# Optimization experiments

Measured on AMD Instinct MI355X. Metric: run time of the kernel, lower is better.

Reference implementation:

```python
import jax, jax.numpy as jnp
import numpy as np

B, C, N, K = 2, 128, 4096, 16
DIM, PH, AH = 256, 64, 1024  # dim, pos_hidden_dim, dim*attn_hidden_multiplier
EPS = 1e-5

def _p(k, shape, scale=0.02):
    return jax.random.normal(k, shape, dtype=jnp.float32) * scale

def setup_inputs() -> dict:
    key0 = jax.random.key(0)
    ks = jax.random.split(key0, 32)
    d = {
        'pos': jax.random.normal(ks[0], (B, 3, N), dtype=jnp.float32),
        'key': jax.random.normal(ks[1], (B, C, N), dtype=jnp.float32),
        'query': jax.random.normal(ks[2], (B, C, N), dtype=jnp.float32),
        # MLP_Res on concat(key,query): in=2C, hidden=C, out=C
        'mlpv_w1': _p(ks[3], (C, 2 * C)), 'mlpv_b1': jnp.zeros((C,)),
        'mlpv_w2': _p(ks[4], (C, C)),     'mlpv_b2': jnp.zeros((C,)),
        'mlpv_ws': _p(ks[5], (C, 2 * C)), 'mlpv_bs': jnp.zeros((C,)),
        'wk': _p(ks[6], (DIM, C)), 'bk': jnp.zeros((DIM,)),
        'wq': _p(ks[7], (DIM, C)), 'bq': jnp.zeros((DIM,)),
        'wv': _p(ks[8], (DIM, C)), 'bv': jnp.zeros((DIM,)),
        # pos_mlp: Conv2d(3,PH,1) -> BN -> ReLU -> Conv2d(PH,DIM,1)
        'pos_w1': _p(ks[9], (PH, 3)),   'pos_b1': jnp.zeros((PH,)),
        'pos_g1': jnp.ones((PH,)),      'pos_be1': jnp.zeros((PH,)),
        'pos_w2': _p(ks[10], (DIM, PH)),'pos_b2': jnp.zeros((DIM,)),
        # attn_mlp: Conv2d(DIM,AH,1) -> BN -> ReLU -> Conv2d(AH,DIM,1)
        'att_w1': _p(ks[11], (AH, DIM)), 'att_b1': jnp.zeros((AH,)),
        'att_g1': jnp.ones((AH,)),       'att_be1': jnp.zeros((AH,)),
        'att_w2': _p(ks[12], (DIM, AH)), 'att_b2': jnp.zeros((DIM,)),
        'we': _p(ks[13], (C, DIM)), 'be': jnp.zeros((C,)),
    }
    return d

def conv1d(w, b, x):  # 1x1 conv: (o,i),(B,i,N)->(B,o,N)
    return jnp.einsum('oi,bin->bon', w, x) + b[None, :, None]

def conv2d(w, b, x):  # 1x1 conv: (o,i),(B,i,N,K)->(B,o,N,K)
    return jnp.einsum('oi,bink->bonk', w, x) + b[None, :, None, None]

def bn2d(g, be, x):  # training-mode batchnorm over (B,N,K) per channel
    m = x.mean(axis=(0, 2, 3), keepdims=True)
    v = x.var(axis=(0, 2, 3), keepdims=True)
    return g[None, :, None, None] * (x - m) * jax.lax.rsqrt(v + EPS) + be[None, :, None, None]

def knn_idx(pos, k):  # pos: (B,3,N) -> idx (B,N,k) of k nearest (incl. self)
    sq = jnp.sum(pos * pos, axis=1)                      # (B,N)
    d2 = sq[:, :, None] + sq[:, None, :] - 2.0 * jnp.einsum('bdn,bdm->bnm', pos, pos)
    _, idx = jax.lax.top_k(-d2, k)                       # smallest distances
    return idx

def group(x, idx):  # x:(B,C,N), idx:(B,N,K) -> (B,C,N,K)
    return jax.vmap(lambda xb, ib: xb[:, ib])(x, idx)

def reference(pos, key, query,
              mlpv_w1, mlpv_b1, mlpv_w2, mlpv_b2, mlpv_ws, mlpv_bs,
              wk, bk, wq, bq, wv, bv,
              pos_w1, pos_b1, pos_g1, pos_be1, pos_w2, pos_b2,
              att_w1, att_b1, att_g1, att_be1, att_w2, att_b2,
              we, be):
    x = jnp.concatenate([key, query], axis=1)            # (B,2C,N)
    value = conv1d(mlpv_w2, mlpv_b2, jax.nn.relu(conv1d(mlpv_w1, mlpv_b1, x))) \
            + conv1d(mlpv_ws, mlpv_bs, x)                # MLP_Res -> (B,C,N)
    identity = value
    k_f = conv1d(wk, bk, key)                            # (B,DIM,N)
    q_f = conv1d(wq, bq, query)
    v_f = conv1d(wv, bv, value)
    idx = knn_idx(pos, K)                                # (B,N,K)
    key_g = group(k_f, idx)                              # (B,DIM,N,K)
    qk_rel = q_f[:, :, :, None] - key_g
    pos_rel = pos[:, :, :, None] - group(pos, idx)       # (B,3,N,K)
    pos_emb = conv2d(pos_w2, pos_b2,
                     jax.nn.relu(bn2d(pos_g1, pos_be1, conv2d(pos_w1, pos_b1, pos_rel))))
    attn = conv2d(att_w2, att_b2,
                  jax.nn.relu(bn2d(att_g1, att_be1, conv2d(att_w1, att_b1, qk_rel + pos_emb))))
    attn = jax.nn.softmax(attn, axis=-1)                 # softmax over K neighbors
    v = v_f[:, :, :, None] + pos_emb                     # (B,DIM,N,K)
    agg = jnp.einsum('bcik,bcik->bci', attn, v)          # (B,DIM,N)
    y = conv1d(we, be, agg)
    return y + identity
```

## Files before the change

### kernel.cpp

```cpp
#include <hip/hip_runtime.h>
#include <math.h>

#define BB 2
#define CC 128
#define NN 4096
#define KK 16
#define DIMD 256
#define PHH 64
#define AHH 1024
#define EPSF 1e-5f
#define RSPLIT 128
#define RKCH ((BB * NN * KK) / RSPLIT)
#define LSTR 258
#define KNN_CAP 512
#define FPT 8

typedef unsigned short ushort_t;
typedef unsigned char uchar_t;
typedef unsigned long long u64;
typedef long long i64;
typedef __attribute__((ext_vector_type(8))) short short8;
typedef __attribute__((ext_vector_type(8))) unsigned short u16x8;
typedef __attribute__((ext_vector_type(4))) unsigned short u16x4;
typedef __attribute__((ext_vector_type(2))) unsigned short u16x2;
typedef __attribute__((ext_vector_type(4))) float f32x4;

__device__ __forceinline__ ushort_t f2b(float x) {
    union { float f; unsigned u; } v; v.f = x;
    unsigned r = v.u + 0x7fff + ((v.u >> 16) & 1);
    return (ushort_t)(r >> 16);
}
__device__ __forceinline__ float b2f(ushort_t x) {
    union { unsigned u; float f; } v; v.u = ((unsigned)x) << 16;
    return v.f;
}
__device__ __forceinline__ unsigned fsort(float x) {
    union { float f; unsigned u; } v; v.f = x;
    return v.u ^ ((v.u >> 31) ? 0xFFFFFFFFu : 0x80000000u);
}
__device__ __forceinline__ uchar_t f2f8(float x) {
    int p = __builtin_amdgcn_cvt_pk_fp8_f32(x, x, 0, false);
    return (uchar_t)(p & 0xFF);
}

#define GLDS16(gp, lp) __builtin_amdgcn_global_load_lds( \
    (const __attribute__((address_space(1))) void*)(gp), \
    (__attribute__((address_space(3))) void*)(lp), 16, 0, 0)

__global__ void zero_kernel(float* p, int n) {
    int i = blockIdx.x * blockDim.x + threadIdx.x;
    if (i < n) p[i] = 0.f;
}

__global__ __launch_bounds__(256) void knn_kernel(const float* __restrict__ pos,
                                                  int* __restrict__ idx) {
    int bid = blockIdx.x;
    int b = bid / NN, n = bid % NN;
    int t = threadIdx.x;
    int lane = t & 63, w = t >> 6;
    const float* px = pos + (size_t)b * 3 * NN;
    const float* py = px + NN;
    const float* pz = px + 2 * NN;
    float qx = px[n], qy = py[n], qz = pz[n];
    float qs = qx * qx + qy * qy + qz * qz;

    u64 keys[KK];
    u64 lmin = ~0ull;
#pragma unroll
    for (int j = 0; j < KK; ++j) {
        int m = t + 256 * j;
        float mx = px[m], my = py[m], mz = pz[m];
        float ms = mx * mx + my * my + mz * mz;
        float dt = qx * mx + qy * my + qz * mz;
        float d = qs + ms - 2.f * dt;
        u64 k = ((u64)fsort(d) << 32) | (unsigned)m;
        keys[j] = k;
        lmin = k < lmin ? k : lmin;
    }

    __shared__ u64 T0s[4];
    __shared__ u64 pool[KNN_CAP];
    __shared__ int cnt;

    u64 k = lmin, m4 = 0;
#pragma unroll
    for (int r = 0; r < 4; ++r) {
        u64 mv = k;
#pragma unroll
        for (int off = 32; off >= 1; off >>= 1) {
            u64 o = __shfl_xor(mv, off);
            mv = o < mv ? o : mv;
        }
        if (r == 3) m4 = mv;
        if (k == mv) k = ~0ull;
    }
    if (lane == 0) T0s[w] = m4;
    if (t == 0) cnt = 0;
    __syncthreads();
    u64 T0 = T0s[0];
    T0 = T0s[1] > T0 ? T0s[1] : T0;
    T0 = T0s[2] > T0 ? T0s[2] : T0;
    T0 = T0s[3] > T0 ? T0s[3] : T0;

#pragma unroll
    for (int j = 0; j < KK; ++j) {
        if (keys[j] <= T0) {
            int p = atomicAdd(&cnt, 1);
            if (p < KNN_CAP) pool[p] = keys[j];
        }
    }
    __syncthreads();
    int C = cnt < KNN_CAP ? cnt : KNN_CAP;
    if (t < C) {
        u64 me = pool[t];
        int r = 0;
        for (int i = 0; i < C; ++i) r += (pool[i] < me);
        if (r < KK) idx[(size_t)bid * KK + r] = (int)(me & 0xFFFFFFFFu);
    }
}

__global__ __launch_bounds__(256) void cvtx_kernel(const float* __restrict__ key,
                                                   const float* __restrict__ query,
                                                   ushort_t* __restrict__ kqT) {
    __shared__ float xs[128][65];
    int b = blockIdx.y, n0 = blockIdx.x * 64, t = threadIdx.x;
    for (int h = 0; h < 2; ++h) {
        const float* src = (h ? query : key) + (size_t)b * CC * NN;
        if (h) __syncthreads();
#pragma unroll
        for (int it = 0; it < 32; ++it) {
            int l = it * 256 + t;
            xs[l >> 6][l & 63] = src[(size_t)(l >> 6) * NN + n0 + (l & 63)];
        }
        __syncthreads();
#pragma unroll
        for (int it = 0; it < 8; ++it) {
            int l = it * 256 + t;
            int row = l >> 5, c0 = (l & 31) * 4;
            u16x4 pk;
            pk[0] = f2b(xs[c0][row]);
            pk[1] = f2b(xs[c0 + 1][row]);
            pk[2] = f2b(xs[c0 + 2][row]);
            pk[3] = f2b(xs[c0 + 3][row]);
            *(u16x4*)(kqT + ((size_t)b * NN + n0 + row) * 256 + h * 128 + c0) = pk;
        }
    }
}

template <int KLOOP, int ASTR, int EPI, int OSTR>
__global__ __launch_bounds__(256) void gemmT_kernel(const ushort_t* __restrict__ A,
                                                    const ushort_t* __restrict__ Bm,
                                                    const float* __restrict__ bias,
                                                    float* __restrict__ outF,
                                                    ushort_t* __restrict__ outB) {
    __shared__ ushort_t lA[128 * 32];
    __shared__ ushort_t lB[128 * 32];
    int t = threadIdx.x, lane = t & 63, w = t >> 6;
    int wr = w >> 1, wc = w & 1;
    size_t row0 = (size_t)blockIdx.x * 128;
    int col0 = blockIdx.y * 128;
    int m16 = lane & 15, kg = lane >> 4;
    f32x4 acc[4][4];
#pragma unroll
    for (int i = 0; i < 4; ++i)
#pragma unroll
        for (int j = 0; j < 4; ++j) acc[i][j] = (f32x4){0.f, 0.f, 0.f, 0.f};

    const ushort_t* gA = A + (row0 + (size_t)w * 16 + m16) * ASTR + kg * 8;
    const ushort_t* gB = Bm + ((size_t)(col0 + w * 16 + m16)) * KLOOP + kg * 8;
    ushort_t* lA0 = lA + w * 512;
    ushort_t* lB0 = lB + w * 512;
    for (int kt = 0; kt < KLOOP / 32; ++kt) {
        int ko = kt * 32;
        GLDS16(gA + ko, lA0);
        GLDS16(gA + (size_t)64 * ASTR + ko, lA0 + 2048);
        GLDS16(gB + ko, lB0);
        GLDS16(gB + (size_t)64 * KLOOP + ko, lB0 + 2048);
        __syncthreads();
        short8 af[4], bf[4];
#pragma unroll
        for (int i = 0; i < 4; ++i) {
            af[i] = *(const short8*)(lA + ((wr * 4 + i) * 512 + kg * 128 + m16 * 8));
            bf[i] = *(const short8*)(lB + ((wc * 4 + i) * 512 + kg * 128 + m16 * 8));
        }
#pragma unroll
        for (int i = 0; i < 4; ++i)
#pragma unroll
            for (int j = 0; j < 4; ++j)
                acc[i][j] = __builtin_amdgcn_mfma_f32_16x16x32_bf16(af[i], bf[j], acc[i][j], 0, 0, 0);
        __syncthreads();
    }
#pragma unroll
    for (int j = 0; j < 4; ++j) {
        int n = col0 + wc * 64 + j * 16 + m16;
        float bi = bias[n];
#pragma unroll
        for (int i = 0; i < 4; ++i) {
            size_t r = row0 + wr * 64 + i * 16 + kg * 4;
#pragma unroll
            for (int rg = 0; rg < 4; ++rg) {
                float v = acc[i][j][rg] + bi;
                if (EPI == 0) outB[(r + rg) * (size_t)OSTR + n] = f2b(fmaxf(v, 0.f));
                else          outF[(r + rg) * (size_t)OSTR + n] = v;
            }
        }
    }
}

__global__ __launch_bounds__(256) void gemmval_kernel(const ushort_t* __restrict__ kqT,
                                                      const ushort_t* __restrict__ h1T,
                                                      const ushort_t* __restrict__ wsb,
                                                      const ushort_t* __restrict__ w2vb,
                                                      const float* __restrict__ b2,
                                                      const float* __restrict__ bs,
                                                      float* __restrict__ valueTf,
                                                      ushort_t* __restrict__ valueTb) {
    __shared__ ushort_t lA[128 * 32];
    __shared__ ushort_t lB[128 * 32];
    int t = threadIdx.x, lane = t & 63, w = t >> 6;
    int wr = w >> 1, wc = w & 1;
    size_t row0 = (size_t)blockIdx.x * 128;
    int m16 = lane & 15, kg = lane >> 4;
    f32x4 acc[4][4];
#pragma unroll
    for (int i = 0; i < 4; ++i)
#pragma unroll
        for (int j = 0; j < 4; ++j) acc[i][j] = (f32x4){0.f, 0.f, 0.f, 0.f};
    ushort_t* lA0 = lA + w * 512;
    ushort_t* lB0 = lB + w * 512;

    {
        const ushort_t* gA = kqT + (row0 + (size_t)w * 16 + m16) * 256 + kg * 8;
        const ushort_t* gB = wsb + ((size_t)(w * 16 + m16)) * 256 + kg * 8;
        for (int kt = 0; kt < 8; ++kt) {
            int ko = kt * 32;
            GLDS16(gA + ko, lA0);
            GLDS16(gA + (size_t)64 * 256 + ko, lA0 + 2048);
            GLDS16(gB + ko, lB0);
            GLDS16(gB + (size_t)64 * 256 + ko, lB0 + 2048);
            __syncthreads();
            short8 af[4], bf[4];
#pragma unroll
            for (int i = 0; i < 4; ++i) {
                af[i] = *(const short8*)(lA + ((wr * 4 + i) * 512 + kg * 128 + m16 * 8));
                bf[i] = *(const short8*)(lB + ((wc * 4 + i) * 512 + kg * 128 + m16 * 8));
            }
#pragma unroll
            for (int i = 0; i < 4; ++i)
#pragma unroll
                for (int j = 0; j < 4; ++j)
                    acc[i][j] = __builtin_amdgcn_mfma_f32_16x16x32_bf16(af[i], bf[j], acc[i][j], 0, 0, 0);
            __syncthreads();
        }
    }
    {
        const ushort_t* gA = h1T + (row0 + (size_t)w * 16 + m16) * 128 + kg * 8;
        const ushort_t* gB = w2vb + ((size_t)(w * 16 + m16)) * 128 + kg * 8;
        for (int kt = 0; kt < 4; ++kt) {
            int ko = kt * 32;
            GLDS16(gA + ko, lA0);
            GLDS16(gA + (size_t)64 * 128 + ko, lA0 + 2048);
            GLDS16(gB + ko, lB0);
            GLDS16(gB + (size_t)64 * 128 + ko, lB0 + 2048);
            __syncthreads();
            short8 af[4], bf[4];
#pragma unroll
            for (int i = 0; i < 4; ++i) {
                af[i] = *(const short8*)(lA + ((wr * 4 + i) * 512 + kg * 128 + m16 * 8));
                bf[i] = *(const short8*)(lB + ((wc * 4 + i) * 512 + kg * 128 + m16 * 8));
            }
#pragma unroll
            for (int i = 0; i < 4; ++i)
#pragma unroll
                for (int j = 0; j < 4; ++j)
                    acc[i][j] = __builtin_amdgcn_mfma_f32_16x16x32_bf16(af[i], bf[j], acc[i][j], 0, 0, 0);
            __syncthreads();
        }
    }
#pragma unroll
    for (int j = 0; j < 4; ++j) {
        int n = wc * 64 + j * 16 + m16;
        float bi = b2[n] + bs[n];
#pragma unroll
        for (int i = 0; i < 4; ++i) {
            size_t r = row0 + wr * 64 + i * 16 + kg * 4;
#pragma unroll
            for (int rg = 0; rg < 4; ++rg) {
                float v = acc[i][j][rg] + bi;
                valueTf[(r + rg) * (size_t)CC + n] = v;
                valueTb[(r + rg) * (size_t)CC + n] = f2b(v);
            }
        }
    }
}

__global__ __launch_bounds__(256) void gemmkq_kernel(const ushort_t* __restrict__ kqT,
                                                     const ushort_t* __restrict__ wkb,
                                                     const ushort_t* __restrict__ wqb,
                                                     const float* __restrict__ bk,
                                                     const float* __restrict__ bq,
                                                     float* __restrict__ kT,
                                                     float* __restrict__ qT) {
    __shared__ ushort_t lA[128 * 32];
    __shared__ ushort_t lB[128 * 32];
    int half = blockIdx.y >> 1;
    int col0 = (blockIdx.y & 1) * 128;
    const ushort_t* A = kqT + half * 128;
    const ushort_t* Bm = half ? wqb : wkb;
    const float* bias = half ? bq : bk;
    float* outF = half ? qT : kT;

    int t = threadIdx.x, lane = t & 63, w = t >> 6;
    int wr = w >> 1, wc = w & 1;
    size_t row0 = (size_t)blockIdx.x * 128;
    int m16 = lane & 15, kg = lane >> 4;
    f32x4 acc[4][4];
#pragma unroll
    for (int i = 0; i < 4; ++i)
#pragma unroll
        for (int j = 0; j < 4; ++j) acc[i][j] = (f32x4){0.f, 0.f, 0.f, 0.f};
    const ushort_t* gA = A + (row0 + (size_t)w * 16 + m16) * 256 + kg * 8;
    const ushort_t* gB = Bm + ((size_t)(col0 + w * 16 + m16)) * 128 + kg * 8;
    ushort_t* lA0 = lA + w * 512;
    ushort_t* lB0 = lB + w * 512;
    for (int kt = 0; kt < 4; ++kt) {
        int ko = kt * 32;
        GLDS16(gA + ko, lA0);
        GLDS16(gA + (size_t)64 * 256 + ko, lA0 + 2048);
        GLDS16(gB + ko, lB0);
        GLDS16(gB + (size_t)64 * 128 + ko, lB0 + 2048);
        __syncthreads();
        short8 af[4], bf[4];
#pragma unroll
        for (int i = 0; i < 4; ++i) {
            af[i] = *(const short8*)(lA + ((wr * 4 + i) * 512 + kg * 128 + m16 * 8));
            bf[i] = *(const short8*)(lB + ((wc * 4 + i) * 512 + kg * 128 + m16 * 8));
        }
#pragma unroll
        for (int i = 0; i < 4; ++i)
#pragma unroll
            for (int j = 0; j < 4; ++j)
                acc[i][j] = __builtin_amdgcn_mfma_f32_16x16x32_bf16(af[i], bf[j], acc[i][j], 0, 0, 0);
        __syncthreads();
    }
#pragma unroll
    for (int j = 0; j < 4; ++j) {
        int n = col0 + wc * 64 + j * 16 + m16;
        float bi = bias[n];
#pragma unroll
        for (int i = 0; i < 4; ++i) {
            size_t r = row0 + wr * 64 + i * 16 + kg * 4;
#pragma unroll
            for (int rg = 0; rg < 4; ++rg)
                outF[(r + rg) * (size_t)DIMD + n] = acc[i][j][rg] + bi;
        }
    }
}

__global__ __launch_bounds__(256) void pos_stats_kernel(const float* __restrict__ pos,
                                                        const int* __restrict__ idx,
                                                        float* __restrict__ stats) {
    int sid = blockIdx.x * 256 + threadIdx.x;
    int b = sid / (NN * KK);
    int r = sid % (NN * KK);
    int n = r / KK;
    int m = idx[sid];
    const float* px = pos + (size_t)b * 3 * NN;
    float dx = px[n] - px[m];
    float dy = px[NN + n] - px[NN + m];
    float dz = px[2 * NN + n] - px[2 * NN + m];
    float v[9] = {dx, dy, dz, dx * dx, dy * dy, dz * dz, dx * dy, dx * dz, dy * dz};
    __shared__ float red[256];
    for (int j = 0; j < 9; ++j) {
        red[threadIdx.x] = v[j];
        __syncthreads();
        for (int off = 128; off >= 1; off >>= 1) {
            if (threadIdx.x < off) red[threadIdx.x] += red[threadIdx.x + off];
            __syncthreads();
        }
        if (threadIdx.x == 0) atomicAdd(&stats[j], red[0]);
        __syncthreads();
    }
}

__global__ void pos_bn_kernel(const float* __restrict__ stats, const float* __restrict__ pw1,
                              const float* __restrict__ pb1, const float* __restrict__ pg1,
                              const float* __restrict__ pbe1, float* __restrict__ posA) {
    int c = threadIdx.x;
    if (c >= PHH) return;
    float M = (float)(BB * NN * KK);
    float mu0 = stats[0] / M, mu1 = stats[1] / M, mu2 = stats[2] / M;
    float E00 = stats[3] / M, E11 = stats[4] / M, E22 = stats[5] / M;
    float E01 = stats[6] / M, E02 = stats[7] / M, E12 = stats[8] / M;
    float w0 = pw1[c * 3], w1 = pw1[c * 3 + 1], w2 = pw1[c * 3 + 2];
    float wmu = w0 * mu0 + w1 * mu1 + w2 * mu2;
    float mean_h = wmu + pb1[c];
    float Eh2 = w0 * w0 * E00 + w1 * w1 * E11 + w2 * w2 * E22
              + 2.f * (w0 * w1 * E01 + w0 * w2 * E02 + w1 * w2 * E12)
              + 2.f * pb1[c] * wmu + pb1[c] * pb1[c];
    float var = Eh2 - mean_h * mean_h;
    float a1 = pg1[c] * rsqrtf(var + EPSF);
    posA[c] = a1;
    posA[PHH + c] = pbe1[c] - mean_h * a1;
}

__global__ __launch_bounds__(256) void p1_kernel(const float* __restrict__ pos,
                                                 const int* __restrict__ idx,
                                                 const float* __restrict__ pw1,
                                                 const float* __restrict__ pb1,
                                                 const float* __restrict__ posA,
                                                 ushort_t* __restrict__ p1) {
    int gid = blockIdx.x * 256 + threadIdx.x;
    int samp = gid >> 6, c = gid & 63;
    int p = samp >> 4;
    int b = p >> 12, n = p & (NN - 1);
    int m = idx[samp];
    const float* px = pos + (size_t)b * 3 * NN;
    float dx = px[n] - px[m];
    float dy = px[NN + n] - px[NN + m];
    float dz = px[2 * NN + n] - px[2 * NN + m];
    float h = pw1[c * 3] * dx + pw1[c * 3 + 1] * dy + pw1[c * 3 + 2] * dz + pb1[c];
    p1[gid] = f2b(fmaxf(h * posA[c] + posA[PHH + c], 0.f));
}

__global__ __launch_bounds__(256) void mu_kernel(const ushort_t* __restrict__ sb16,
                                                 float* __restrict__ mu) {
    __shared__ float red[8][DIMD];
    int t = threadIdx.x;
    int rg = t >> 5;
    int c0 = (t & 31) * 8;
    const ushort_t* p = sb16 + ((size_t)blockIdx.x * 512 + rg * 64) * DIMD + c0;
    float a0 = 0.f, a1 = 0.f, a2 = 0.f, a3 = 0.f, a4 = 0.f, a5 = 0.f, a6 = 0.f, a7 = 0.f;
    for (int i = 0; i < 64; ++i) {
        u16x8 v = *(const u16x8*)(p + (size_t)i * DIMD);
        a0 += b2f(v[0]); a1 += b2f(v[1]); a2 += b2f(v[2]); a3 += b2f(v[3]);
        a4 += b2f(v[4]); a5 += b2f(v[5]); a6 += b2f(v[6]); a7 += b2f(v[7]);
    }
    red[rg][c0] = a0; red[rg][c0 + 1] = a1; red[rg][c0 + 2] = a2; red[rg][c0 + 3] = a3;
    red[rg][c0 + 4] = a4; red[rg][c0 + 5] = a5; red[rg][c0 + 6] = a6; red[rg][c0 + 7] = a7;
    __syncthreads();
    float s = 0.f;
#pragma unroll
    for (int g = 0; g < 8; ++g) s += red[g][t];
    atomicAdd(&mu[t], s);
}

__global__ __launch_bounds__(256) void rg_kernel(const ushort_t* __restrict__ S,
                                                 float* __restrict__ Rpart) {
    __shared__ ushort_t ls[32 * LSTR];
    int t = threadIdx.x;
    int lane = t & 63, w = t >> 6;
    int wr = w >> 1, wc = w & 1;
    int ti = blockIdx.y >> 1, tj = blockIdx.y & 1;
    int m16 = lane & 15, kg = lane >> 4;
    size_t kbase = (size_t)blockIdx.x * RKCH;

    f32x4 acc[4][4];
#pragma unroll
    for (int i = 0; i < 4; ++i)
#pragma unroll
        for (int j = 0; j < 4; ++j) acc[i][j] = (f32x4){0.f, 0.f, 0.f, 0.f};

    int lm = t >> 3;
    int lc = (t & 7) * 32;
    const ushort_t* gS = S + (kbase + lm) * DIMD + lc;
    ushort_t* lp = ls + lm * LSTR + lc;

    for (int kt = 0; kt < RKCH / 32; ++kt) {
        const ushort_t* gp = gS + (size_t)kt * 32 * DIMD;
        u16x8 v0 = *(const u16x8*)(gp);
        u16x8 v1 = *(const u16x8*)(gp + 8);
        u16x8 v2 = *(const u16x8*)(gp + 16);
        u16x8 v3 = *(const u16x8*)(gp + 24);
        __syncthreads();
#pragma unroll
        for (int q = 0; q < 4; ++q) {
            *(u16x2*)(lp + 0 + 2 * q) = (u16x2){v0[2 * q], v0[2 * q + 1]};
            *(u16x2*)(lp + 8 + 2 * q) = (u16x2){v1[2 * q], v1[2 * q + 1]};
            *(u16x2*)(lp + 16 + 2 * q) = (u16x2){v2[2 * q], v2[2 * q + 1]};
            *(u16x2*)(lp + 24 + 2 * q) = (u16x2){v3[2 * q], v3[2 * q + 1]};
        }
        __syncthreads();
        short8 af[4], bf[4];
#pragma unroll
        for (int i = 0; i < 4; ++i) {
            int chA = ti * 128 + wr * 64 + i * 16 + m16;
            int chB = tj * 128 + wc * 64 + i * 16 + m16;
#pragma unroll
            for (int j = 0; j < 8; ++j) {
                int k = kg * 8 + j;
                af[i][j] = (short)ls[k * LSTR + chA];
                bf[i][j] = (short)ls[k * LSTR + chB];
            }
        }
#pragma unroll
        for (int i = 0; i < 4; ++i)
#pragma unroll
            for (int j = 0; j < 4; ++j)
                acc[i][j] = __builtin_amdgcn_mfma_f32_16x16x32_bf16(af[i], bf[j], acc[i][j], 0, 0, 0);
    }

    float* rp = Rpart + (size_t)blockIdx.x * (DIMD * DIMD);
#pragma unroll
    for (int i = 0; i < 4; ++i) {
        int r0 = ti * 128 + wr * 64 + i * 16 + kg * 4;
#pragma unroll
        for (int j = 0; j < 4; ++j) {
            int cn = tj * 128 + wc * 64 + j * 16 + m16;
#pragma unroll
            for (int rg = 0; rg < 4; ++rg)
                rp[(size_t)(r0 + rg) * DIMD + cn] = acc[i][j][rg];
        }
    }
}

__global__ __launch_bounds__(256) void r_reduce_kernel(const float* __restrict__ Rpart,
                                                       float* __restrict__ R) {
    int e = blockIdx.x * 256 + threadIdx.x;
    float s = 0.f;
    for (int p = 0; p < RSPLIT; ++p) s += Rpart[(size_t)p * (DIMD * DIMD) + e];
    R[e] = s;
}

__global__ __launch_bounds__(256) void attn_bn_kernel(const float* __restrict__ R,
                                                      const float* __restrict__ mu,
                                                      const float* __restrict__ aw1,
                                                      const float* __restrict__ ab1,
                                                      const float* __restrict__ ag1,
                                                      const float* __restrict__ abe1,
                                                      float* __restrict__ attA) {
    int c = blockIdx.x;
    int t = threadIdx.x;
    __shared__ float wsh[DIMD];
    __shared__ float red[DIMD];
    wsh[t] = aw1[(size_t)c * DIMD + t];
    __syncthreads();
    const float* Rr = R + (size_t)t * DIMD;
    float q = 0.f;
#pragma unroll 4
    for (int j = 0; j < DIMD; ++j) q += Rr[j] * wsh[j];
    red[t] = q * wsh[t];
    __syncthreads();
    for (int off = 128; off >= 1; off >>= 1) {
        if (t < off) red[t] += red[t + off];
        __syncthreads();
    }
    float wRw = red[0];
    __syncthreads();
    red[t] = wsh[t] * mu[t];
    __syncthreads();
    for (int off = 128; off >= 1; off >>= 1) {
        if (t < off) red[t] += red[t + off];
        __syncthreads();
    }
    if (t == 0) {
        float M = (float)(BB * NN * KK);
        float wmu = red[0] / M;
        float b1c = ab1[c];
        float Eh = wmu + b1c;
        float Eh2 = wRw / M + 2.f * b1c * wmu + b1c * b1c;
        float var = Eh2 - Eh * Eh;
        float a1 = ag1[c] * rsqrtf(var + EPSF);
        attA[c] = a1;
        attA[AHH + c] = a1 * b1c + abe1[c] - Eh * a1;
    }
}

__global__ void cvt_w_kernel(const float* __restrict__ aw1, const float* __restrict__ aw2,
                             const float* __restrict__ pw2,
                             const float* __restrict__ mw1, const float* __restrict__ mws,
                             const float* __restrict__ mw2,
                             const float* __restrict__ wk, const float* __restrict__ wq,
                             const float* __restrict__ wv,
                             ushort_t* __restrict__ w1b, ushort_t* __restrict__ w2b,
                             ushort_t* __restrict__ pw2b,
                             ushort_t* __restrict__ w1vb, ushort_t* __restrict__ wsvb,
                             ushort_t* __restrict__ w2vb,
                             ushort_t* __restrict__ wkb, ushort_t* __restrict__ wqb,
                             ushort_t* __restrict__ wvb,
                             uchar_t* __restrict__ w2f8) {
    int i = blockIdx.x * 256 + threadIdx.x;
    int o = i;
    if (o < 262144) { w1b[o] = f2b(aw1[o]); return; }   o -= 262144;
    if (o < 262144) { w2b[o] = f2b(aw2[o]); w2f8[o] = f2f8(aw2[o] * 64.f); return; } o -= 262144;
    if (o < 16384)  { pw2b[o] = f2b(pw2[o]); return; }  o -= 16384;
    if (o < 32768)  { w1vb[o] = f2b(mw1[o]); return; }  o -= 32768;
    if (o < 32768)  { wsvb[o] = f2b(mws[o]); return; }  o -= 32768;
    if (o < 16384)  { w2vb[o] = f2b(mw2[o]); return; }  o -= 16384;
    if (o < 32768)  { wkb[o] = f2b(wk[o]); return; }    o -= 32768;
    if (o < 32768)  { wqb[o] = f2b(wq[o]); return; }    o -= 32768;
    if (o < 32768)  { wvb[o] = f2b(wv[o]); }
}

template <int KDIM>
__global__ __launch_bounds__(256) void gemmS_kernel(const ushort_t* __restrict__ A,
                                                    const ushort_t* __restrict__ Bm,
                                                    const float* __restrict__ p0,
                                                    ushort_t* __restrict__ Sb,
                                                    const float* __restrict__ qT,
                                                    const float* __restrict__ kT,
                                                    const int* __restrict__ gidx) {
    __shared__ ushort_t lA[128 * 32];
    __shared__ ushort_t lB[128 * 32];
    int t = threadIdx.x;
    int lane = t & 63, w = t >> 6;
    int wr = w >> 1, wc = w & 1;
    size_t row0 = (size_t)blockIdx.x * 128;
    int col0 = blockIdx.y * 128;
    int m16 = lane & 15, kg = lane >> 4;

    f32x4 acc[4][4];
#pragma unroll
    for (int i = 0; i < 4; ++i)
#pragma unroll
        for (int j = 0; j < 4; ++j) acc[i][j] = (f32x4){0.f, 0.f, 0.f, 0.f};

    const ushort_t* gA = A + (row0 + (size_t)w * 16 + m16) * KDIM + kg * 8;
    const ushort_t* gB = Bm + ((size_t)(col0 + w * 16 + m16)) * KDIM + kg * 8;
    ushort_t* lA0 = lA + w * 512;
    ushort_t* lB0 = lB + w * 512;

    for (int kt = 0; kt < KDIM / 32; ++kt) {
        int ko = kt * 32;
        GLDS16(gA + ko, lA0);
        GLDS16(gA + (size_t)64 * KDIM + ko, lA0 + 2048);
        GLDS16(gB + ko, lB0);
        GLDS16(gB + (size_t)64 * KDIM + ko, lB0 + 2048);
        __syncthreads();
        short8 af[4], bf[4];
#pragma unroll
        for (int i = 0; i < 4; ++i) {
            af[i] = *(const short8*)(lA + ((wr * 4 + i) * 512 + kg * 128 + m16 * 8));
            bf[i] = *(const short8*)(lB + ((wc * 4 + i) * 512 + kg * 128 + m16 * 8));
        }
#pragma unroll
        for (int i = 0; i < 4; ++i)
#pragma unroll
            for (int j = 0; j < 4; ++j)
                acc[i][j] = __builtin_amdgcn_mfma_f32_16x16x32_bf16(af[i], bf[j], acc[i][j], 0, 0, 0);
        __syncthreads();
    }

    int nn[4]; float bi[4];
#pragma unroll
    for (int j = 0; j < 4; ++j) { nn[j] = col0 + wc * 64 + j * 16 + m16; bi[j] = p0[nn[j]]; }
#pragma unroll
    for (int i = 0; i < 4; ++i) {
        size_t r = row0 + wr * 64 + i * 16 + kg * 4;
#pragma unroll
        for (int rg = 0; rg < 4; ++rg) {
            size_t rr = r + rg;
            int p = (int)(rr >> 4);
            int krow = (p & ~(NN - 1)) + gidx[rr];
            const float* qrow = qT + (size_t)p * DIMD;
            const float* kro = kT + (size_t)krow * DIMD;
#pragma unroll
            for (int j = 0; j < 4; ++j) {
                float sv = qrow[nn[j]] - kro[nn[j]] + acc[i][j][rg] + bi[j];
                Sb[rr * (size_t)DIMD + nn[j]] = f2b(sv);
            }
        }
    }
}

__global__ __launch_bounds__(256, 3) void fused_mlp_kernel(const ushort_t* __restrict__ S,
                                                        const ushort_t* __restrict__ w1b,
                                                        const uchar_t* __restrict__ w2f8,
                                                        const float* __restrict__ attA,
                                                        const float* __restrict__ ab2,
                                                        const int* __restrict__ idx,
                                                        const float* __restrict__ qT,
                                                        const float* __restrict__ kT,
                                                        const float* __restrict__ vT,
                                                        float* __restrict__ aggT) {
    __shared__ char smem[49152];
    ushort_t* lS  = (ushort_t*)smem;
    uchar_t*  lHt = (uchar_t*)(smem + 32768);
    ushort_t* lgB = (ushort_t*)smem;

    int t = threadIdx.x;
    int lane = t & 63, w = t >> 6;
    int m16 = lane & 15, kg = lane >> 4;
    size_t row0 = (size_t)blockIdx.x * 64;

#pragma unroll
    for (int i = 0; i < 8; ++i) {
        int lb = w * 8 + i;
        int kt = lb >> 2, st = lb & 3;
        const ushort_t* gp = S + (row0 + st * 16 + m16) * DIMD + kt * 32 + kg * 8;
        GLDS16(gp, lS + lb * 512);
    }

    f32x4 acc2[4][4];
#pragma unroll
    for (int i = 0; i < 4; ++i)
#pragma unroll
        for (int j = 0; j < 4; ++j) acc2[i][j] = (f32x4){0.f, 0.f, 0.f, 0.f};

    __syncthreads();

    for (int jc = 0; jc < 8; ++jc) {
        uchar_t* lHb = lHt + (jc & 1) * 8192;
        f32x4 acc1[2][4];
#pragma unroll
        for (int hi = 0; hi < 2; ++hi)
#pragma unroll
            for (int sj = 0; sj < 4; ++sj) acc1[hi][sj] = (f32x4){0.f, 0.f, 0.f, 0.f};
        const ushort_t* wrow = w1b + ((size_t)(jc * 128 + w * 32 + m16)) * DIMD + kg * 8;
#pragma unroll
        for (int kt = 0; kt < 8; ++kt) {
            short8 af[2], bf[4];
            af[0] = *(const short8*)(wrow + kt * 32);
            af[1] = *(const short8*)(wrow + (size_t)16 * DIMD + kt * 32);
#pragma unroll
            for (int sj = 0; sj < 4; ++sj)
                bf[sj] = *(const short8*)(lS + (kt * 4 + sj) * 512 + kg * 128 + m16 * 8);
            __builtin_amdgcn_s_setprio(1);
#pragma unroll
            for (int hi = 0; hi < 2; ++hi)
#pragma unroll
                for (int sj = 0; sj < 4; ++sj)
                    acc1[hi][sj] = __builtin_amdgcn_mfma_f32_16x16x32_bf16(af[hi], bf[sj], acc1[hi][sj], 0, 0, 0);
            __builtin_amdgcn_s_setprio(0);
        }
#pragma unroll
        for (int hi = 0; hi < 2; ++hi) {
            float4 sc4 = *(const float4*)(attA + jc * 128 + w * 32 + hi * 16 + kg * 4);
            float4 of4 = *(const float4*)(attA + AHH + jc * 128 + w * 32 + hi * 16 + kg * 4);
#pragma unroll
            for (int sj = 0; sj < 4; ++sj) {
                float h0 = fmaxf(sc4.x * acc1[hi][sj][0] + of4.x, 0.f);
                float h1 = fmaxf(sc4.y * acc1[hi][sj][1] + of4.y, 0.f);
                float h2 = fmaxf(sc4.z * acc1[hi][sj][2] + of4.z, 0.f);
                float h3 = fmaxf(sc4.w * acc1[hi][sj][3] + of4.w, 0.f);
                int p01 = __builtin_amdgcn_cvt_pk_fp8_f32(h0, h1, 0, false);
                int pk = __builtin_amdgcn_cvt_pk_fp8_f32(h2, h3, p01, true);
                int ah = (w * 4 + sj) * 512 + (hi * 2 + (kg >> 1)) * 128 + m16 * 8 + (kg & 1) * 4;
                *(int*)(lHb + ah) = pk;
            }
        }
        __syncthreads();
#pragma unroll
        for (int gh = 0; gh < 2; ++gh) {
            i64 af2[8];
#pragma unroll
            for (int gq = 0; gq < 2; ++gq)
#pragma unroll
                for (int oi = 0; oi < 4; ++oi)
                    af2[gq * 4 + oi] = *(const i64*)(w2f8 + ((size_t)(w * 64 + oi * 16 + m16)) * AHH + jc * 128 + (gh * 2 + gq) * 32 + kg * 8);
#pragma unroll
            for (int gq = 0; gq < 2; ++gq) {
                i64 bf2[4];
#pragma unroll
                for (int sj = 0; sj < 4; ++sj)
                    bf2[sj] = *(const i64*)(lHb + ((gh * 2 + gq) * 4 + sj) * 512 + kg * 128 + m16 * 8);
                __builtin_amdgcn_s_setprio(1);
#pragma unroll
                for (int oi = 0; oi < 4; ++oi)
#pragma unroll
                    for (int sj = 0; sj < 4; ++sj)
                        acc2[oi][sj] = __builtin_amdgcn_mfma_f32_16x16x32_fp8_fp8(af2[gq * 4 + oi], bf2[sj], acc2[oi][sj], 0, 0, 0);
                __builtin_amdgcn_s_setprio(0);
            }
        }
    }
    __syncthreads();

    const float invsc = 0.015625f;
#pragma unroll
    for (int oi = 0; oi < 4; ++oi) {
        int ob = w * 64 + oi * 16 + kg * 4;
        float4 b2v = *(const float4*)(ab2 + ob);
#pragma unroll
        for (int sj = 0; sj < 4; ++sj) {
            int smp = sj * 16 + m16;
            lgB[(ob + 0) * 72 + smp] = f2b(acc2[oi][sj][0] * invsc + b2v.x);
            lgB[(ob + 1) * 72 + smp] = f2b(acc2[oi][sj][1] * invsc + b2v.y);
            lgB[(ob + 2) * 72 + smp] = f2b(acc2[oi][sj][2] * invsc + b2v.z);
            lgB[(ob + 3) * 72 + smp] = f2b(acc2[oi][sj][3] * invsc + b2v.w);
        }
    }
    __syncthreads();

    int out = t;
    for (int pt = 0; pt < 4; ++pt) {
        int pid = (int)(row0 >> 4) + pt;
        u16x8 v0 = *(const u16x8*)(lgB + out * 72 + pt * 16);
        u16x8 v1 = *(const u16x8*)(lgB + out * 72 + pt * 16 + 8);
        float lg[KK];
#pragma unroll
        for (int s = 0; s < 8; ++s) { lg[s] = b2f(v0[s]); lg[s + 8] = b2f(v1[s]); }
        float mx = lg[0];
#pragma unroll
        for (int s = 1; s < KK; ++s) mx = fmaxf(mx, lg[s]);
        float se = 0.f;
#pragma unroll
        for (int s = 0; s < KK; ++s) { lg[s] = expf(lg[s] - mx); se += lg[s]; }
        float inv = 1.f / se;
        int base = pid & ~(NN - 1);
        float acc = 0.f;
#pragma unroll
        for (int s = 0; s < KK; ++s) {
            int row = pid * KK + s;
            int krow = base + idx[row];
            float sv = b2f(S[(size_t)row * DIMD + out]);
            float kv = kT[(size_t)krow * DIMD + out];
            acc += lg[s] * (sv + kv);
        }
        float vf = vT[(size_t)pid * DIMD + out];
        float q  = qT[(size_t)pid * DIMD + out];
        aggT[(size_t)pid * DIMD + out] = vf - q + acc * inv;
    }
}

__global__ __launch_bounds__(256) void final_kernel(const float* __restrict__ aggT,
                                                    const float* __restrict__ we,
                                                    const float* __restrict__ be,
                                                    const float* __restrict__ valueTf,
                                                    float* __restrict__ out) {
    __shared__ float xs[2 * FPT][DIMD];
    __shared__ float vs[2 * FPT][CC];
    int b = blockIdx.y;
    int n0 = blockIdx.x * (2 * FPT);
    int t = threadIdx.x;
    const float4* src = (const float4*)(aggT + ((size_t)b * NN + n0) * DIMD);
    float4* dst = (float4*)xs;
#pragma unroll
    for (int l = 0; l < (2 * FPT * DIMD / 4) / 256; ++l) dst[t + 256 * l] = src[t + 256 * l];
    const float4* src2 = (const float4*)(valueTf + ((size_t)b * NN + n0) * CC);
    float4* dst2 = (float4*)vs;
#pragma unroll
    for (int l = 0; l < (2 * FPT * CC / 4) / 256; ++l) dst2[t + 256 * l] = src2[t + 256 * l];
    __syncthreads();
    int o = t & 127, ph = t >> 7;
    float acc[FPT];
#pragma unroll
    for (int p = 0; p < FPT; ++p) acc[p] = 0.f;
    const float4* wr = (const float4*)(we + (size_t)o * DIMD);
#pragma unroll 8
    for (int i4 = 0; i4 < DIMD / 4; ++i4) {
        float4 w4 = wr[i4];
#pragma unroll
        for (int p = 0; p < FPT; ++p) {
            float4 x4 = *(const float4*)&xs[ph * FPT + p][i4 * 4];
            acc[p] += w4.x * x4.x + w4.y * x4.y + w4.z * x4.z + w4.w * x4.w;
        }
    }
    float bo = be[o];
#pragma unroll
    for (int p = 0; p < FPT; ++p) {
        size_t oi = ((size_t)b * CC + o) * NN + n0 + ph * FPT + p;
        out[oi] = acc[p] + bo + vs[ph * FPT + p][o];
    }
}

extern "C" void kernel_launch(void* const* d_in, const int* in_sizes, int n_in,
                              void* d_out, int out_size, void* d_ws, size_t ws_size,
                              hipStream_t stream) {
    (void)in_sizes; (void)n_in; (void)out_size; (void)ws_size;
    const float* pos     = (const float*)d_in[0];
    const float* key     = (const float*)d_in[1];
    const float* query   = (const float*)d_in[2];
    const float* mlpv_w1 = (const float*)d_in[3];
    const float* mlpv_b1 = (const float*)d_in[4];
    const float* mlpv_w2 = (const float*)d_in[5];
    const float* mlpv_b2 = (const float*)d_in[6];
    const float* mlpv_ws = (const float*)d_in[7];
    const float* mlpv_bs = (const float*)d_in[8];
    const float* wk  = (const float*)d_in[9];
    const float* bk  = (const float*)d_in[10];
    const float* wq  = (const float*)d_in[11];
    const float* bq  = (const float*)d_in[12];
    const float* wv  = (const float*)d_in[13];
    const float* bv  = (const float*)d_in[14];
    const float* pw1 = (const float*)d_in[15];
    const float* pb1 = (const float*)d_in[16];
    const float* pg1 = (const float*)d_in[17];
    const float* pbe1= (const float*)d_in[18];
    const float* pw2 = (const float*)d_in[19];
    const float* pb2 = (const float*)d_in[20];
    const float* aw1 = (const float*)d_in[21];
    const float* ab1 = (const float*)d_in[22];
    const float* ag1 = (const float*)d_in[23];
    const float* abe1= (const float*)d_in[24];
    const float* aw2 = (const float*)d_in[25];
    const float* ab2 = (const float*)d_in[26];
    const float* we  = (const float*)d_in[27];
    const float* be  = (const float*)d_in[28];
    float* out = (float*)d_out;

    char* wsb = (char*)d_ws;
    size_t off = 0;
    auto alloc = [&](size_t bytes) {
        void* p = wsb + off;
        off += (bytes + 255) & ~(size_t)255;
        return p;
    };
    const size_t M = (size_t)BB * NN * KK;
    const size_t P = (size_t)BB * NN;
    int*   idx   = (int*)  alloc(M * 4);
    ushort_t* kqT     = (ushort_t*)alloc(P * 256 * 2);
    ushort_t* h1T     = (ushort_t*)alloc(P * CC * 2);
    float*    valueTf = (float*)   alloc(P * CC * 4);
    ushort_t* valueTb = (ushort_t*)alloc(P * CC * 2);
    float* kT    = (float*)alloc(P * DIMD * 4);
    float* qT    = (float*)alloc(P * DIMD * 4);
    float* vT    = (float*)alloc(P * DIMD * 4);
    float* aggT  = (float*)alloc(P * DIMD * 4);
    float* zero0 = (float*)alloc((size_t)(16 + 256 + 65536) * 4);
    float* stats = zero0;
    float* mu    = zero0 + 16;
    float* R     = zero0 + 16 + 256;
    float* posA  = (float*)alloc((size_t)2 * PHH * 4);
    float* attA  = (float*)alloc((size_t)2 * AHH * 4);
    ushort_t* w1b  = (ushort_t*)alloc((size_t)AHH * DIMD * 2);
    ushort_t* w2b  = (ushort_t*)alloc((size_t)DIMD * AHH * 2);
    uchar_t*  w2f8 = (uchar_t*) alloc((size_t)DIMD * AHH);
    ushort_t* pw2b = (ushort_t*)alloc((size_t)DIMD * PHH * 2);
    ushort_t* w1vb = (ushort_t*)alloc((size_t)CC * 256 * 2);
    ushort_t* wsvb = (ushort_t*)alloc((size_t)CC * 256 * 2);
    ushort_t* w2vb = (ushort_t*)alloc((size_t)CC * CC * 2);
    ushort_t* wkb  = (ushort_t*)alloc((size_t)DIMD * CC * 2);
    ushort_t* wqb  = (ushort_t*)alloc((size_t)DIMD * CC * 2);
    ushort_t* wvb  = (ushort_t*)alloc((size_t)DIMD * CC * 2);
    ushort_t* sb16 = (ushort_t*)alloc(M * DIMD * 2);
    char* ovl = (char*)alloc((size_t)RSPLIT * DIMD * DIMD * 4);
    ushort_t* p1buf = (ushort_t*)ovl;
    float*    Rpart = (float*)ovl;

    int ZN = 16 + 256 + 65536;
    zero_kernel<<<(ZN + 255) / 256, 256, 0, stream>>>(zero0, ZN);
    knn_kernel<<<BB * NN, 256, 0, stream>>>(pos, idx);
    cvt_w_kernel<<<(720896 + 255) / 256, 256, 0, stream>>>(aw1, aw2, pw2, mlpv_w1, mlpv_ws, mlpv_w2,
                                                           wk, wq, wv, w1b, w2b, pw2b,
                                                           w1vb, wsvb, w2vb, wkb, wqb, wvb, w2f8);
    cvtx_kernel<<<dim3(NN / 64, BB), 256, 0, stream>>>(key, query, kqT);
    gemmT_kernel<256, 256, 0, 128><<<dim3(P / 128, 1), 256, 0, stream>>>(kqT, w1vb, mlpv_b1, nullptr, h1T);
    gemmval_kernel<<<dim3(P / 128, 1), 256, 0, stream>>>(kqT, h1T, wsvb, w2vb, mlpv_b2, mlpv_bs, valueTf, valueTb);
    gemmkq_kernel<<<dim3(P / 128, 4), 256, 0, stream>>>(kqT, wkb, wqb, bk, bq, kT, qT);
    gemmT_kernel<128, 128, 1, 256><<<dim3(P / 128, 2), 256, 0, stream>>>(valueTb, wvb, bv, vT, nullptr);
    pos_stats_kernel<<<BB * NN * KK / 256, 256, 0, stream>>>(pos, idx, stats);
    pos_bn_kernel<<<1, 64, 0, stream>>>(stats, pw1, pb1, pg1, pbe1, posA);
    p1_kernel<<<(int)(M * PHH / 256), 256, 0, stream>>>(pos, idx, pw1, pb1, posA, p1buf);
    gemmS_kernel<PHH><<<dim3(M / 128, DIMD / 128), 256, 0, stream>>>(p1buf, pw2b, pb2, sb16, qT, kT, idx);
    mu_kernel<<<(int)(M / 512), 256, 0, stream>>>(sb16, mu);
    rg_kernel<<<dim3(RSPLIT, 4), 256, 0, stream>>>(sb16, Rpart);
    r_reduce_kernel<<<DIMD * DIMD / 256, 256, 0, stream>>>(Rpart, R);
    attn_bn_kernel<<<AHH, DIMD, 0, stream>>>(R, mu, aw1, ab1, ag1, abe1, attA);
    fused_mlp_kernel<<<(int)(M / 64), 256, 0, stream>>>(sb16, w1b, w2f8, attA, ab2, idx, qT, kT, vT, aggT);
    final_kernel<<<dim3(NN / (2 * FPT), BB), 256, 0, stream>>>(aggT, we, be, valueTf, out);
}
```

Baseline: 685.0 us.

## Split softmax-aggregation out of fused MLP kernel into separate kernel

New measurement: 737.6 us. 7.7% more time.

```diff
diff --git a/kernel.cpp b/kernel.cpp
--- a/kernel.cpp
+++ b/kernel.cpp
@@ -14,6 +14,7 @@
 #define LSTR 258
 #define KNN_CAP 512
 #define FPT 8
+#define MM (BB * NN * KK)
 
 typedef unsigned short ushort_t;
 typedef unsigned char uchar_t;
@@ -668,11 +669,7 @@
                                                         const uchar_t* __restrict__ w2f8,
                                                         const float* __restrict__ attA,
                                                         const float* __restrict__ ab2,
-                                                        const int* __restrict__ idx,
-                                                        const float* __restrict__ qT,
-                                                        const float* __restrict__ kT,
-                                                        const float* __restrict__ vT,
-                                                        float* __restrict__ aggT) {
+                                                        ushort_t* __restrict__ lgG) {
     __shared__ char smem[49152];
     ushort_t* lS  = (ushort_t*)smem;
     uchar_t*  lHt = (uchar_t*)(smem + 32768);
@@ -782,11 +779,40 @@
     }
     __syncthreads();
 
+    {
+        ushort_t* dst = lgG + (size_t)t * MM + row0;
+#pragma unroll
+        for (int i = 0; i < 8; ++i) {
+            u16x8 v = *(const u16x8*)(lgB + t * 72 + i * 8);
+            *(u16x8*)(dst + i * 8) = v;
+        }
+    }
+}
+
+__global__ __launch_bounds__(256) void softagg_kernel(const ushort_t* __restrict__ lgG,
+                                                      const ushort_t* __restrict__ S,
+                                                      const int* __restrict__ idx,
+                                                      const float* __restrict__ qT,
+                                                      const float* __restrict__ kT,
+                                                      const float* __restrict__ vT,
+                                                      float* __restrict__ aggT) {
+    __shared__ ushort_t lS2[64 * DIMD];
+    int t = threadIdx.x;
+    size_t r0 = (size_t)blockIdx.x * 64;
+
+    const u16x8* srcv = (const u16x8*)(S + r0 * DIMD);
+    u16x8* dstv = (u16x8*)lS2;
+#pragma unroll
+    for (int i = 0; i < 8; ++i) dstv[i * 256 + t] = srcv[i * 256 + t];
+    __syncthreads();
+
     int out = t;
+    int pid0 = blockIdx.x * 4;
     for (int pt = 0; pt < 4; ++pt) {
-        int pid = (int)(row0 >> 4) + pt;
-        u16x8 v0 = *(const u16x8*)(lgB + out * 72 + pt * 16);
-        u16x8 v1 = *(const u16x8*)(lgB + out * 72 + pt * 16 + 8);
+        int pid = pid0 + pt;
+        const ushort_t* lgp = lgG + (size_t)out * MM + (size_t)pid * KK;
+        u16x8 v0 = *(const u16x8*)(lgp);
+        u16x8 v1 = *(const u16x8*)(lgp + 8);
         float lg[KK];
 #pragma unroll
         for (int s = 0; s < 8; ++s) { lg[s] = b2f(v0[s]); lg[s + 8] = b2f(v1[s]); }
@@ -803,7 +829,7 @@
         for (int s = 0; s < KK; ++s) {
             int row = pid * KK + s;
             int krow = base + idx[row];
-            float sv = b2f(S[(size_t)row * DIMD + out]);
+            float sv = b2f(lS2[(pt * 16 + s) * DIMD + out]);
             float kv = kT[(size_t)krow * DIMD + out];
             acc += lg[s] * (sv + kv);
         }
@@ -924,9 +950,10 @@
     ushort_t* wqb  = (ushort_t*)alloc((size_t)DIMD * CC * 2);
     ushort_t* wvb  = (ushort_t*)alloc((size_t)DIMD * CC * 2);
     ushort_t* sb16 = (ushort_t*)alloc(M * DIMD * 2);
-    char* ovl = (char*)alloc((size_t)RSPLIT * DIMD * DIMD * 4);
+    char* ovl = (char*)alloc(M * DIMD * 2);
     ushort_t* p1buf = (ushort_t*)ovl;
     float*    Rpart = (float*)ovl;
+    ushort_t* lgG   = (ushort_t*)ovl;
 
     int ZN = 16 + 256 + 65536;
     zero_kernel<<<(ZN + 255) / 256, 256, 0, stream>>>(zero0, ZN);
@@ -947,6 +974,7 @@
     rg_kernel<<<dim3(RSPLIT, 4), 256, 0, stream>>>(sb16, Rpart);
     r_reduce_kernel<<<DIMD * DIMD / 256, 256, 0, stream>>>(Rpart, R);
     attn_bn_kernel<<<AHH, DIMD, 0, stream>>>(R, mu, aw1, ab1, ag1, abe1, attA);
-    fused_mlp_kernel<<<(int)(M / 64), 256, 0, stream>>>(sb16, w1b, w2f8, attA, ab2, idx, qT, kT, vT, aggT);
+    fused_mlp_kernel<<<(int)(M / 64), 256, 0, stream>>>(sb16, w1b, w2f8, attA, ab2, lgG);
+    softagg_kernel<<<(int)(M / 64), 256, 0, stream>>>(lgG, sb16, idx, qT, kT, vT, aggT);
     final_kernel<<<dim3(NN / (2 * FPT), BB), 256, 0, stream>>>(aggT, we, be, valueTf, out);
 }
```

## Fuse column-mean reduction into Gram kernel and cover all output tiles per block

Applied to the files above, without the earlier changes.

Measured after the change: 685.8 us. No clear change (+0.1%).

```diff
diff --git a/kernel.cpp b/kernel.cpp
--- a/kernel.cpp
+++ b/kernel.cpp
@@ -9,7 +9,7 @@
 #define PHH 64
 #define AHH 1024
 #define EPSF 1e-5f
-#define RSPLIT 128
+#define RSPLIT 256
 #define RKCH ((BB * NN * KK) / RSPLIT)
 #define LSTR 258
 #define KNN_CAP 512
@@ -423,63 +423,42 @@
     p1[gid] = f2b(fmaxf(h * posA[c] + posA[PHH + c], 0.f));
 }
 
-__global__ __launch_bounds__(256) void mu_kernel(const ushort_t* __restrict__ sb16,
-                                                 float* __restrict__ mu) {
-    __shared__ float red[8][DIMD];
-    int t = threadIdx.x;
-    int rg = t >> 5;
-    int c0 = (t & 31) * 8;
-    const ushort_t* p = sb16 + ((size_t)blockIdx.x * 512 + rg * 64) * DIMD + c0;
-    float a0 = 0.f, a1 = 0.f, a2 = 0.f, a3 = 0.f, a4 = 0.f, a5 = 0.f, a6 = 0.f, a7 = 0.f;
-    for (int i = 0; i < 64; ++i) {
-        u16x8 v = *(const u16x8*)(p + (size_t)i * DIMD);
-        a0 += b2f(v[0]); a1 += b2f(v[1]); a2 += b2f(v[2]); a3 += b2f(v[3]);
-        a4 += b2f(v[4]); a5 += b2f(v[5]); a6 += b2f(v[6]); a7 += b2f(v[7]);
-    }
-    red[rg][c0] = a0; red[rg][c0 + 1] = a1; red[rg][c0 + 2] = a2; red[rg][c0 + 3] = a3;
-    red[rg][c0 + 4] = a4; red[rg][c0 + 5] = a5; red[rg][c0 + 6] = a6; red[rg][c0 + 7] = a7;
-    __syncthreads();
-    float s = 0.f;
-#pragma unroll
-    for (int g = 0; g < 8; ++g) s += red[g][t];
-    atomicAdd(&mu[t], s);
-}
-
-__global__ __launch_bounds__(256) void rg_kernel(const ushort_t* __restrict__ S,
-                                                 float* __restrict__ Rpart) {
+__global__ __launch_bounds__(1024) void rg_kernel(const ushort_t* __restrict__ S,
+                                                  float* __restrict__ Rpart,
+                                                  float* __restrict__ mu) {
     __shared__ ushort_t ls[32 * LSTR];
+    __shared__ float fmu[DIMD];
     int t = threadIdx.x;
     int lane = t & 63, w = t >> 6;
-    int wr = w >> 1, wc = w & 1;
-    int ti = blockIdx.y >> 1, tj = blockIdx.y & 1;
+    int ti = w >> 3, tj = (w >> 2) & 1;
+    int wr = (w >> 1) & 1, wc = w & 1;
     int m16 = lane & 15, kg = lane >> 4;
     size_t kbase = (size_t)blockIdx.x * RKCH;
 
+    if (t < DIMD) fmu[t] = 0.f;
+
     f32x4 acc[4][4];
 #pragma unroll
     for (int i = 0; i < 4; ++i)
 #pragma unroll
         for (int j = 0; j < 4; ++j) acc[i][j] = (f32x4){0.f, 0.f, 0.f, 0.f};
 
-    int lm = t >> 3;
-    int lc = (t & 7) * 32;
+    int lm = t >> 5;
+    int lc = (t & 31) * 8;
     const ushort_t* gS = S + (kbase + lm) * DIMD + lc;
     ushort_t* lp = ls + lm * LSTR + lc;
+    float csum[8];
+#pragma unroll
+    for (int c = 0; c < 8; ++c) csum[c] = 0.f;
 
     for (int kt = 0; kt < RKCH / 32; ++kt) {
-        const ushort_t* gp = gS + (size_t)kt * 32 * DIMD;
-        u16x8 v0 = *(const u16x8*)(gp);
-        u16x8 v1 = *(const u16x8*)(gp + 8);
-        u16x8 v2 = *(const u16x8*)(gp + 16);
-        u16x8 v3 = *(const u16x8*)(gp + 24);
-        __syncthreads();
-#pragma unroll
-        for (int q = 0; q < 4; ++q) {
-            *(u16x2*)(lp + 0 + 2 * q) = (u16x2){v0[2 * q], v0[2 * q + 1]};
-            *(u16x2*)(lp + 8 + 2 * q) = (u16x2){v1[2 * q], v1[2 * q + 1]};
-            *(u16x2*)(lp + 16 + 2 * q) = (u16x2){v2[2 * q], v2[2 * q + 1]};
-            *(u16x2*)(lp + 24 + 2 * q) = (u16x2){v3[2 * q], v3[2 * q + 1]};
-        }
+        u16x8 v = *(const u16x8*)(gS + (size_t)kt * 32 * DIMD);
+        __syncthreads();
+#pragma unroll
+        for (int q = 0; q < 4; ++q)
+            *(u16x2*)(lp + 2 * q) = (u16x2){v[2 * q], v[2 * q + 1]};
+#pragma unroll
+        for (int c = 0; c < 8; ++c) csum[c] += b2f(v[c]);
         __syncthreads();
         short8 af[4], bf[4];
 #pragma unroll
@@ -512,6 +491,12 @@
                 rp[(size_t)(r0 + rg) * DIMD + cn] = acc[i][j][rg];
         }
     }
+
+    __syncthreads();
+#pragma unroll
+    for (int c = 0; c < 8; ++c) atomicAdd(&fmu[lc + c], csum[c]);
+    __syncthreads();
+    if (t < DIMD) atomicAdd(&mu[t], fmu[t]);
 }
 
 __global__ __launch_bounds__(256) void r_reduce_kernel(const float* __restrict__ Rpart,
@@ -924,7 +909,7 @@
     ushort_t* wqb  = (ushort_t*)alloc((size_t)DIMD * CC * 2);
     ushort_t* wvb  = (ushort_t*)alloc((size_t)DIMD * CC * 2);
     ushort_t* sb16 = (ushort_t*)alloc(M * DIMD * 2);
-    char* ovl = (char*)alloc((size_t)RSPLIT * DIMD * DIMD * 4);
+    char* ovl = (char*)alloc(M * DIMD * 2);
     ushort_t* p1buf = (ushort_t*)ovl;
     float*    Rpart = (float*)ovl;
 
@@ -943,8 +928,7 @@
     pos_bn_kernel<<<1, 64, 0, stream>>>(stats, pw1, pb1, pg1, pbe1, posA);
     p1_kernel<<<(int)(M * PHH / 256), 256, 0, stream>>>(pos, idx, pw1, pb1, posA, p1buf);
     gemmS_kernel<PHH><<<dim3(M / 128, DIMD / 128), 256, 0, stream>>>(p1buf, pw2b, pb2, sb16, qT, kT, idx);
-    mu_kernel<<<(int)(M / 512), 256, 0, stream>>>(sb16, mu);
-    rg_kernel<<<dim3(RSPLIT, 4), 256, 0, stream>>>(sb16, Rpart);
+    rg_kernel<<<RSPLIT, 1024, 0, stream>>>(sb16, Rpart, mu);
     r_reduce_kernel<<<DIMD * DIMD / 256, 256, 0, stream>>>(Rpart, R);
     attn_bn_kernel<<<AHH, DIMD, 0, stream>>>(R, mu, aw1, ab1, ag1, abe1, attA);
     fused_mlp_kernel<<<(int)(M / 64), 256, 0, stream>>>(sb16, w1b, w2f8, attA, ab2, idx, qT, kT, vT, aggT);
```
